# Performance work log

Hardware: AMD Instinct MI355X
Metric: run time of the kernel (lower is better)

Reference implementation:

```python
import jax, jax.numpy as jnp
import numpy as np

OUT_F, IN_F = 4096, 4096
N_FREQ = 10000
SCALING = 150.0


def iwht(x):
    """Unnormalized fast Walsh-Hadamard transform along axis 0. x: [n, m], n power of 2."""
    n, m = x.shape
    steps = int(np.log2(n))
    x = x.reshape((2,) * steps + (m,))
    for ax in range(steps):  # log2(n) butterfly stages
        a, b = jnp.split(x, 2, axis=ax)
        x = jnp.concatenate([a + b, a - b], axis=ax)
    return x.reshape(n, m)


def setup_inputs() -> dict:
    key = jax.random.key(0)
    k1, k2, k3, k4 = jax.random.split(key, 4)
    x = jax.random.normal(k1, (2, 512, IN_F), dtype=jnp.float32)
    weight = jax.random.normal(k2, (OUT_F, IN_F), dtype=jnp.float32) * 0.02
    spectrum = jax.random.normal(k3, (N_FREQ,), dtype=jnp.float32)
    indices = jax.random.randint(k4, (2, N_FREQ), 0, OUT_F, dtype=jnp.int64)
    return {"x": x, "weight": weight, "spectrum": spectrum, "indices": indices}


def reference(x, weight, spectrum, indices):
    out_f, in_f = weight.shape
    # sparse scatter of spectrum into dense (out, in) matrix
    dense = jnp.zeros((out_f, in_f), dtype=spectrum.dtype).at[indices[0], indices[1]].set(spectrum)
    # inverse WHT along out axis, scaled
    delta_w = iwht(dense) * (SCALING / np.sqrt(np.float32(out_f)))
    # F.linear(x, base_w + delta_w)
    return jnp.einsum('bsi,oi->bso', x, weight + delta_w.astype(x.dtype))
```

## Files before the change

kernel.cpp:

```cpp
#include <hip/hip_runtime.h>

typedef unsigned short ushort_t;

#define M_DIM 1024
#define N_DIM 4096
#define K_DIM 4096
#define NFREQ 10000
constexpr float SCALE = 150.0f / 64.0f;

typedef __bf16 bf16x8_t __attribute__((ext_vector_type(8)));
typedef float  f32x4_t  __attribute__((ext_vector_type(4)));

__device__ inline ushort_t f2bf(float f) {
  union { float f; unsigned u; } v; v.f = f;
  unsigned r = v.u + 0x7fffu + ((v.u >> 16) & 1u);
  return (ushort_t)(r >> 16);
}

__global__ __launch_bounds__(256) void build_w3(
    const float* __restrict__ weight,
    const float* __restrict__ spectrum,
    const int* __restrict__ idx,
    ushort_t* __restrict__ wb) {
  constexpr int CAP = 1024;
  __shared__ unsigned e_raw[CAP];
  __shared__ float    v_raw[CAP];
  __shared__ unsigned e_srt[CAP];
  __shared__ float    v_srt[CAP];
  __shared__ int cnt;
  __shared__ int cstart[65];
  __shared__ int coff[64];
  __shared__ int ccnt[64];

  const int tid = threadIdx.x;
  const int ci0 = blockIdx.x * 64;
  const int o0  = blockIdx.y * 256;

  if (tid == 0) cnt = 0;
  if (tid < 64) ccnt[tid] = 0;
  __syncthreads();

  for (int j = tid; j < NFREQ; j += 256) {
    int c = idx[NFREQ + j];
    if ((c >> 6) == (int)blockIdx.x) {
      int p = atomicAdd(&cnt, 1);
      if (p < CAP) {
        e_raw[p] = ((unsigned)(c & 63) << 26) | ((unsigned)j << 12) | (unsigned)idx[j];
        v_raw[p] = spectrum[j];
        atomicAdd(&ccnt[c & 63], 1);
      }
    }
  }
  __syncthreads();
  const int n = cnt < CAP ? cnt : CAP;

  if (tid < 64) {
    int v = ccnt[tid];
    int s = v;
    for (int d = 1; d < 64; d <<= 1) {
      int o = __shfl_up(s, d, 64);
      if (tid >= d) s += o;
    }
    cstart[tid + 1] = s;
    if (tid == 0) cstart[0] = 0;
    coff[tid] = s - v;
  }
  __syncthreads();
  for (int e = tid; e < n; e += 256) {
    unsigned w = e_raw[e];
    int dc = w >> 26;
    int p = atomicAdd(&coff[dc], 1);
    e_srt[p] = w;
    v_srt[p] = v_raw[e];
  }
  __syncthreads();

  for (int e = tid; e < n; e += 256) {
    unsigned w = e_srt[e];
    int dc = w >> 26;
    unsigned r = w & 0xFFFu, j = (w >> 12) & 0x3FFFu;
    int s0 = cstart[dc], e0 = cstart[dc + 1];
    bool dead = false;
    for (int p = s0; p < e0; ++p) {
      unsigned w2 = e_srt[p];
      if ((w2 & 0xFFFu) == r && ((w2 >> 12) & 0x3FFFu) > j) dead = true;
    }
    if (dead) v_srt[e] = 0.0f;
  }
  __syncthreads();

  const int dc0 = (tid & 15) * 4;
  const int rof = tid >> 4;
  const int s0 = cstart[dc0],     e0 = cstart[dc0 + 1];
  const int s1 = cstart[dc0 + 1], e1 = cstart[dc0 + 2];
  const int s2 = cstart[dc0 + 2], e2 = cstart[dc0 + 3];
  const int s3 = cstart[dc0 + 3], e3 = cstart[dc0 + 4];

  size_t g = (size_t)(o0 + rof) * K_DIM + ci0 + dc0;
  float4 w4 = *(const float4*)&weight[g];
  for (int pass = 0; pass < 16; ++pass) {
    size_t gn = g + (size_t)16 * K_DIM;
    float4 wnext;
    if (pass < 15) wnext = *(const float4*)&weight[gn];
    int o = o0 + pass * 16 + rof;
    float a0 = 0.f, a1 = 0.f, a2 = 0.f, a3 = 0.f;
    for (int p = s0; p < e0; ++p) { float v = v_srt[p]; a0 += (__popc(o & (e_srt[p] & 0xFFFu)) & 1) ? -v : v; }
    for (int p = s1; p < e1; ++p) { float v = v_srt[p]; a1 += (__popc(o & (e_srt[p] & 0xFFFu)) & 1) ? -v : v; }
    for (int p = s2; p < e2; ++p) { float v = v_srt[p]; a2 += (__popc(o & (e_srt[p] & 0xFFFu)) & 1) ? -v : v; }
    for (int p = s3; p < e3; ++p) { float v = v_srt[p]; a3 += (__popc(o & (e_srt[p] & 0xFFFu)) & 1) ? -v : v; }
    ushort4 ov;
    ov.x = f2bf(w4.x + SCALE * a0);
    ov.y = f2bf(w4.y + SCALE * a1);
    ov.z = f2bf(w4.z + SCALE * a2);
    ov.w = f2bf(w4.w + SCALE * a3);
    *(ushort4*)&wb[g] = ov;
    w4 = wnext;
    g = gn;
  }
}

__global__ __launch_bounds__(256) void cvt_x(const float* __restrict__ x,
                                             ushort_t* __restrict__ xb) {
  int i = blockIdx.x * 256 + threadIdx.x;
  float4 v = ((const float4*)x)[i];
  ushort4 o;
  o.x = f2bf(v.x); o.y = f2bf(v.y); o.z = f2bf(v.z); o.w = f2bf(v.w);
  ((ushort4*)xb)[i] = o;
}

__global__ __launch_bounds__(256) void gemm_bt(
    const ushort_t* __restrict__ A,
    const ushort_t* __restrict__ B,
    float* __restrict__ C0,
    float* __restrict__ C1,
    int klen) {
  constexpr int BM = 128, BN = 128, BK = 64;
  __shared__ __align__(16) ushort_t As[BM * BK];
  __shared__ __align__(16) ushort_t Bs[BN * BK];

  const int tid  = threadIdx.x;
  const int wave = tid >> 6, lane = tid & 63;
  const int wrow = wave >> 1, wcol = wave & 1;
  const int l16  = lane & 15, quad = lane >> 4;
  const int bm = blockIdx.y * BM, bn = blockIdx.x * BN;
  const int kbeg = blockIdx.z * klen;
  float* __restrict__ dst = blockIdx.z ? C1 : C0;

  const int srow8 = lane >> 3;
  const int sq    = lane & 7;

  f32x4_t acc[4][4] = {};

  for (int kt = kbeg; kt < kbeg + klen; kt += BK) {
#pragma unroll
    for (int c = 0; c < 4; ++c) {
      int ch = wave * 4 + c;
      int gr = ch * 8 + srow8;
      int qg = sq ^ (gr & 7);
      const ushort_t* ga = A + (size_t)(bm + gr) * K_DIM + kt + qg * 8;
      __builtin_amdgcn_global_load_lds(
          (const __attribute__((address_space(1))) void*)ga,
          (__attribute__((address_space(3))) void*)&As[ch * 512], 16, 0, 0);
      const ushort_t* gb = B + (size_t)(bn + gr) * K_DIM + kt + qg * 8;
      __builtin_amdgcn_global_load_lds(
          (const __attribute__((address_space(1))) void*)gb,
          (__attribute__((address_space(3))) void*)&Bs[ch * 512], 16, 0, 0);
    }
    __syncthreads();

    bf16x8_t af[2][4], bfr[2][4];
#pragma unroll
    for (int h = 0; h < 2; ++h) {
#pragma unroll
      for (int i = 0; i < 4; ++i) {
        int kq = h * 4 + quad;
        int ar = wrow * 64 + i * 16 + l16;
        af[h][i]  = *(const bf16x8_t*)&As[ar * BK + ((kq ^ (ar & 7)) * 8)];
        int br = wcol * 64 + i * 16 + l16;
        bfr[h][i] = *(const bf16x8_t*)&Bs[br * BK + ((kq ^ (br & 7)) * 8)];
      }
    }
#pragma unroll
    for (int h = 0; h < 2; ++h)
#pragma unroll
      for (int i = 0; i < 4; ++i)
#pragma unroll
        for (int j = 0; j < 4; ++j)
          acc[i][j] = __builtin_amdgcn_mfma_f32_16x16x32_bf16(af[h][i], bfr[h][j], acc[i][j], 0, 0, 0);
    __syncthreads();
  }

#pragma unroll
  for (int i = 0; i < 4; ++i) {
#pragma unroll
    for (int j = 0; j < 4; ++j) {
      int col = bn + wcol * 64 + j * 16 + l16;
#pragma unroll
      for (int r = 0; r < 4; ++r) {
        int row = bm + wrow * 64 + i * 16 + quad * 4 + r;
        dst[(size_t)row * N_DIM + col] = acc[i][j][r];
      }
    }
  }
}

__global__ __launch_bounds__(256) void add_partial(float* __restrict__ out,
                                                   const float* __restrict__ part) {
  int i = blockIdx.x * 256 + threadIdx.x;
  float4 a = ((const float4*)out)[i];
  float4 b = ((const float4*)part)[i];
  a.x += b.x; a.y += b.y; a.z += b.z; a.w += b.w;
  ((float4*)out)[i] = a;
}

extern "C" void kernel_launch(void* const* d_in, const int* in_sizes, int n_in,
                              void* d_out, int out_size, void* d_ws, size_t ws_size,
                              hipStream_t stream) {
  const float* x        = (const float*)d_in[0];
  const float* weight   = (const float*)d_in[1];
  const float* spectrum = (const float*)d_in[2];
  const int*   indices  = (const int*)d_in[3];
  float* out = (float*)d_out;

  char* ws = (char*)d_ws;
  const size_t WB_BYTES   = (size_t)N_DIM * K_DIM * 2;
  const size_t XB_BYTES   = (size_t)M_DIM * K_DIM * 2;
  const size_t PART_BYTES = (size_t)M_DIM * N_DIM * 4;

  ushort_t* wb = (ushort_t*)ws;
  ushort_t* xb = (ushort_t*)(ws + WB_BYTES);
  const bool split = ws_size >= WB_BYTES + XB_BYTES + PART_BYTES;
  float* part = (float*)(ws + WB_BYTES + XB_BYTES);

  build_w3<<<dim3(K_DIM / 64, N_DIM / 256), 256, 0, stream>>>(weight, spectrum, indices, wb);
  cvt_x<<<(M_DIM * K_DIM / 4) / 256, 256, 0, stream>>>(x, xb);

  if (split) {
    gemm_bt<<<dim3(N_DIM / 128, M_DIM / 128, 2), 256, 0, stream>>>(xb, wb, out, part, K_DIM / 2);
    add_partial<<<(M_DIM * N_DIM / 4) / 256, 256, 0, stream>>>(out, part);
  } else {
    gemm_bt<<<dim3(N_DIM / 128, M_DIM / 128, 1), 256, 0, stream>>>(xb, wb, out, out, K_DIM);
  }
}
```

Before: 203.6 us.

## Fuse x conversion into weight build, batch Walsh rows, allow 4-way split-K

```diff
diff --git a/kernel.cpp b/kernel.cpp
--- a/kernel.cpp
+++ b/kernel.cpp
@@ -17,20 +17,35 @@
   return (ushort_t)(r >> 16);
 }
 
-__global__ __launch_bounds__(256) void build_w3(
+__global__ __launch_bounds__(256) void build_w4(
     const float* __restrict__ weight,
     const float* __restrict__ spectrum,
     const int* __restrict__ idx,
-    ushort_t* __restrict__ wb) {
+    const float* __restrict__ x,
+    ushort_t* __restrict__ wb,
+    ushort_t* __restrict__ xb) {
+  if (blockIdx.y == 16) {
+    int flat = blockIdx.x * 256 + threadIdx.x;
+#pragma unroll 4
+    for (int k = 0; k < 64; ++k) {
+      int i = flat + k * 16384;
+      float4 v = ((const float4*)x)[i];
+      ushort4 o;
+      o.x = f2bf(v.x); o.y = f2bf(v.y); o.z = f2bf(v.z); o.w = f2bf(v.w);
+      ((ushort4*)xb)[i] = o;
+    }
+    return;
+  }
+
   constexpr int CAP = 1024;
   __shared__ unsigned e_raw[CAP];
   __shared__ float    v_raw[CAP];
-  __shared__ unsigned e_srt[CAP];
-  __shared__ float    v_srt[CAP];
+  __shared__ uint2    ev_srt[CAP];
   __shared__ int cnt;
   __shared__ int cstart[65];
   __shared__ int coff[64];
   __shared__ int ccnt[64];
+  __shared__ unsigned walsh16[16];
 
   const int tid = threadIdx.x;
   const int ci0 = blockIdx.x * 64;
@@ -38,6 +53,12 @@
 
   if (tid == 0) cnt = 0;
   if (tid < 64) ccnt[tid] = 0;
+  if (tid < 16) {
+    unsigned m = tid;
+    unsigned w = (m & 1 ? 0xAAAAu : 0u) ^ (m & 2 ? 0xCCCCu : 0u)
+               ^ (m & 4 ? 0xF0F0u : 0u) ^ (m & 8 ? 0xFF00u : 0u);
+    walsh16[m] = w;
+  }
   __syncthreads();
 
   for (int j = tid; j < NFREQ; j += 256) {
@@ -70,62 +91,61 @@
     unsigned w = e_raw[e];
     int dc = w >> 26;
     int p = atomicAdd(&coff[dc], 1);
-    e_srt[p] = w;
-    v_srt[p] = v_raw[e];
+    ev_srt[p] = make_uint2(w, __float_as_uint(v_raw[e]));
   }
   __syncthreads();
 
   for (int e = tid; e < n; e += 256) {
-    unsigned w = e_srt[e];
-    int dc = w >> 26;
-    unsigned r = w & 0xFFFu, j = (w >> 12) & 0x3FFFu;
+    uint2 ev = ev_srt[e];
+    int dc = ev.x >> 26;
+    unsigned r = ev.x & 0xFFFu, j = (ev.x >> 12) & 0x3FFFu;
     int s0 = cstart[dc], e0 = cstart[dc + 1];
     bool dead = false;
     for (int p = s0; p < e0; ++p) {
-      unsigned w2 = e_srt[p];
+      unsigned w2 = ev_srt[p].x;
       if ((w2 & 0xFFFu) == r && ((w2 >> 12) & 0x3FFFu) > j) dead = true;
     }
-    if (dead) v_srt[e] = 0.0f;
-  }
-  __syncthreads();
-
-  const int dc0 = (tid & 15) * 4;
-  const int rof = tid >> 4;
-  const int s0 = cstart[dc0],     e0 = cstart[dc0 + 1];
-  const int s1 = cstart[dc0 + 1], e1 = cstart[dc0 + 2];
-  const int s2 = cstart[dc0 + 2], e2 = cstart[dc0 + 3];
-  const int s3 = cstart[dc0 + 3], e3 = cstart[dc0 + 4];
-
-  size_t g = (size_t)(o0 + rof) * K_DIM + ci0 + dc0;
-  float4 w4 = *(const float4*)&weight[g];
-  for (int pass = 0; pass < 16; ++pass) {
-    size_t gn = g + (size_t)16 * K_DIM;
-    float4 wnext;
-    if (pass < 15) wnext = *(const float4*)&weight[gn];
-    int o = o0 + pass * 16 + rof;
-    float a0 = 0.f, a1 = 0.f, a2 = 0.f, a3 = 0.f;
-    for (int p = s0; p < e0; ++p) { float v = v_srt[p]; a0 += (__popc(o & (e_srt[p] & 0xFFFu)) & 1) ? -v : v; }
-    for (int p = s1; p < e1; ++p) { float v = v_srt[p]; a1 += (__popc(o & (e_srt[p] & 0xFFFu)) & 1) ? -v : v; }
-    for (int p = s2; p < e2; ++p) { float v = v_srt[p]; a2 += (__popc(o & (e_srt[p] & 0xFFFu)) & 1) ? -v : v; }
-    for (int p = s3; p < e3; ++p) { float v = v_srt[p]; a3 += (__popc(o & (e_srt[p] & 0xFFFu)) & 1) ? -v : v; }
+    if (dead) ev_srt[e].y = 0u;
+  }
+  __syncthreads();
+
+  const int dc0   = (tid & 15) * 4;
+  const int rof   = tid >> 4;
+  const int obase = o0 + rof * 16;
+
+  float acc[4][16];
+#pragma unroll
+  for (int c = 0; c < 4; ++c)
+#pragma unroll
+    for (int j = 0; j < 16; ++j) acc[c][j] = 0.0f;
+
+#pragma unroll
+  for (int c = 0; c < 4; ++c) {
+    const int s = cstart[dc0 + c], e = cstart[dc0 + c + 1];
+    for (int p = s; p < e; ++p) {
+      uint2 ev = ev_srt[p];
+      unsigned r = ev.x & 0xFFFu;
+      unsigned W = walsh16[r & 15u];
+      unsigned sx = ev.y ^ ((unsigned)(__popc(obase & r) & 1) << 31);
+#pragma unroll
+      for (int j = 0; j < 16; ++j) {
+        acc[c][j] += __uint_as_float(sx ^ ((W << (31 - j)) & 0x80000000u));
+      }
+    }
+  }
+
+  size_t g = (size_t)obase * K_DIM + ci0 + dc0;
+#pragma unroll 4
+  for (int j = 0; j < 16; ++j) {
+    float4 w4 = *(const float4*)&weight[g];
     ushort4 ov;
-    ov.x = f2bf(w4.x + SCALE * a0);
-    ov.y = f2bf(w4.y + SCALE * a1);
-    ov.z = f2bf(w4.z + SCALE * a2);
-    ov.w = f2bf(w4.w + SCALE * a3);
+    ov.x = f2bf(w4.x + SCALE * acc[0][j]);
+    ov.y = f2bf(w4.y + SCALE * acc[1][j]);
+    ov.z = f2bf(w4.z + SCALE * acc[2][j]);
+    ov.w = f2bf(w4.w + SCALE * acc[3][j]);
     *(ushort4*)&wb[g] = ov;
-    w4 = wnext;
-    g = gn;
-  }
-}
-
-__global__ __launch_bounds__(256) void cvt_x(const float* __restrict__ x,
-                                             ushort_t* __restrict__ xb) {
-  int i = blockIdx.x * 256 + threadIdx.x;
-  float4 v = ((const float4*)x)[i];
-  ushort4 o;
-  o.x = f2bf(v.x); o.y = f2bf(v.y); o.z = f2bf(v.z); o.w = f2bf(v.w);
-  ((ushort4*)xb)[i] = o;
+    g += K_DIM;
+  }
 }
 
 __global__ __launch_bounds__(256) void gemm_bt(
@@ -144,7 +164,8 @@
   const int l16  = lane & 15, quad = lane >> 4;
   const int bm = blockIdx.y * BM, bn = blockIdx.x * BN;
   const int kbeg = blockIdx.z * klen;
-  float* __restrict__ dst = blockIdx.z ? C1 : C0;
+  float* __restrict__ dst = blockIdx.z == 0
+      ? C0 : C1 + (size_t)(blockIdx.z - 1) * M_DIM * N_DIM;
 
   const int srow8 = lane >> 3;
   const int sq    = lane & 7;
@@ -204,12 +225,15 @@
   }
 }
 
-__global__ __launch_bounds__(256) void add_partial(float* __restrict__ out,
-                                                   const float* __restrict__ part) {
+__global__ __launch_bounds__(256) void reduce_n(float* __restrict__ out,
+                                                const float* __restrict__ part,
+                                                int npart) {
   int i = blockIdx.x * 256 + threadIdx.x;
   float4 a = ((const float4*)out)[i];
-  float4 b = ((const float4*)part)[i];
-  a.x += b.x; a.y += b.y; a.z += b.z; a.w += b.w;
+  for (int t = 0; t < npart; ++t) {
+    float4 b = ((const float4*)(part + (size_t)t * M_DIM * N_DIM))[i];
+    a.x += b.x; a.y += b.y; a.z += b.z; a.w += b.w;
+  }
   ((float4*)out)[i] = a;
 }
 
@@ -223,22 +247,23 @@
   float* out = (float*)d_out;
 
   char* ws = (char*)d_ws;
-  const size_t WB_BYTES   = (size_t)N_DIM * K_DIM * 2;
-  const size_t XB_BYTES   = (size_t)M_DIM * K_DIM * 2;
-  const size_t PART_BYTES = (size_t)M_DIM * N_DIM * 4;
+  const size_t WB_BYTES = (size_t)N_DIM * K_DIM * 2;
+  const size_t XB_BYTES = (size_t)M_DIM * K_DIM * 2;
+  const size_t P1_BYTES = (size_t)M_DIM * N_DIM * 4;
 
   ushort_t* wb = (ushort_t*)ws;
   ushort_t* xb = (ushort_t*)(ws + WB_BYTES);
-  const bool split = ws_size >= WB_BYTES + XB_BYTES + PART_BYTES;
   float* part = (float*)(ws + WB_BYTES + XB_BYTES);
 
-  build_w3<<<dim3(K_DIM / 64, N_DIM / 256), 256, 0, stream>>>(weight, spectrum, indices, wb);
-  cvt_x<<<(M_DIM * K_DIM / 4) / 256, 256, 0, stream>>>(x, xb);
-
-  if (split) {
-    gemm_bt<<<dim3(N_DIM / 128, M_DIM / 128, 2), 256, 0, stream>>>(xb, wb, out, part, K_DIM / 2);
-    add_partial<<<(M_DIM * N_DIM / 4) / 256, 256, 0, stream>>>(out, part);
-  } else {
-    gemm_bt<<<dim3(N_DIM / 128, M_DIM / 128, 1), 256, 0, stream>>>(xb, wb, out, out, K_DIM);
-  }
-}
+  int zsplit;
+  if (ws_size >= WB_BYTES + XB_BYTES + 3 * P1_BYTES)      zsplit = 4;
+  else if (ws_size >= WB_BYTES + XB_BYTES + P1_BYTES)     zsplit = 2;
+  else                                                    zsplit = 1;
+
+  build_w4<<<dim3(64, 17), 256, 0, stream>>>(weight, spectrum, indices, x, wb, xb);
+
+  gemm_bt<<<dim3(N_DIM / 128, M_DIM / 128, zsplit), 256, 0, stream>>>(
+      xb, wb, out, part, K_DIM / zsplit);
+  if (zsplit > 1)
+    reduce_n<<<(M_DIM * N_DIM / 4) / 256, 256, 0, stream>>>(out, part, zsplit - 1);
+}
```

Measured after the change: 226.1 us. 11.0% more time.
